# Kernel tuning notes

Hardware: AMD Instinct MI355X
Metric: run time of the kernel (lower is better)

## Reference

```python
import jax, jax.numpy as jnp
import numpy as np

B, L, W, H = 16, 256, 4, 128
N = L + W - 1  # 259
EPS = 1e-6


def setup_inputs() -> dict:
    key = jax.random.key(0)
    k1, k2 = jax.random.split(key)
    x1 = jax.random.normal(k1, (B, 1, N, H), dtype=jnp.float32)
    x2 = jax.random.normal(k2, (B, 1, N, H), dtype=jnp.float32)
    return {"x1": x1, "x2": x2}


def _attention_matrix(x1, x2):
    # x1: (B,1,n,d); x2.permute(0,2,1,3): (B,n,1,d) -> broadcast diff (B,n,n,d)
    diff = x1 - jnp.transpose(x2, (0, 2, 1, 3))
    euclid = jnp.sqrt(jnp.sum(diff * diff, axis=3) + EPS)  # (B,n,n)
    return 1.0 / (euclid + 1.0)


def _wp(x, a):
    # x: (B,1,n,H), a: (B,n) -> weighted sliding-window sum over W positions
    wx = x * a[:, None, :, None]  # (B,1,n,H)
    out = wx[:, :, 0:L, :]
    for k in range(1, W):  # small fixed loop over filter width
        out = out + wx[:, :, k:k + L, :]
    return out  # (B,1,L,H)


def reference(x1, x2):
    att = _attention_matrix(x1, x2)      # (B,n,n)
    x1_a = jnp.sum(att, axis=1)          # (B,n) weight per x1 position
    x2_a = jnp.sum(att, axis=2)          # (B,n) weight per x2 position
    return (_wp(x1, x1_a), _wp(x2, x2_a))
```

## Files before the change

kernel.cpp:

```cpp
#include <hip/hip_runtime.h>
#include <math.h>

#define Bn  16
#define Ln  256
#define Wn  4
#define Hn  128
#define Nn  259
#define EPSF 1e-6f
#define NB  (Bn * Nn)

#define STR 132


__global__ __launch_bounds__(256) void prep(const float* __restrict__ x1,
                                            const float* __restrict__ x2,
                                            float* __restrict__ ws) {
    const int wid  = (blockIdx.x * 256 + threadIdx.x) >> 6;
    const int lane = threadIdx.x & 63;
    if (wid >= 2 * NB) return;
    const float* x = (wid < NB) ? x1 : x2;
    const int    r = (wid < NB) ? wid : wid - NB;
    const float2 v = ((const float2*)(x + (size_t)r * Hn))[lane];
    float s = v.x * v.x + v.y * v.y;
    #pragma unroll
    for (int off = 32; off; off >>= 1) s += __shfl_down(s, off);
    if (lane == 0) {
        ws[wid]          = 0.f;
        ws[2 * NB + wid] = s;
    }
}

__global__ __launch_bounds__(256, 3) void att_sums(const float* __restrict__ x1,
                                                   const float* __restrict__ x2,
                                                   float* __restrict__ ws) {
    __shared__ float x2t[32 * STR];
    __shared__ float x1t[64 * STR];
    __shared__ float nrm[96];

    float*       x1a = ws;
    float*       x2a = ws + NB;
    const float* n1g = ws + 2 * NB;
    const float* n2g = ws + 3 * NB;

    const int b   = blockIdx.z;
    const int i0  = blockIdx.x * 32;
    const int j0  = blockIdx.y * 64;
    const int tid = threadIdx.x;
    const int ti2 = tid >> 4;
    const int tjg = tid & 15;

    const float* __restrict__ x1b = x1 + (size_t)b * Nn * Hn;
    const float* __restrict__ x2b = x2 + (size_t)b * Nn * Hn;

    for (int idx = tid; idx < 32 * 32; idx += 256) {
        const int r = idx >> 5, c = idx & 31;
        float4 v = make_float4(0.f, 0.f, 0.f, 0.f);
        if (i0 + r < Nn) v = ((const float4*)(x2b + (i0 + r) * Hn))[c];
        *((float4*)&x2t[r * STR + c * 4]) = v;
    }
    for (int idx = tid; idx < 64 * 32; idx += 256) {
        const int r = idx >> 5, c = idx & 31;
        float4 v = make_float4(0.f, 0.f, 0.f, 0.f);
        if (j0 + r < Nn) v = ((const float4*)(x1b + (j0 + r) * Hn))[c];
        *((float4*)&x1t[r * STR + c * 4]) = v;
    }
    if (tid < 32)       nrm[tid]      = (i0 + tid < Nn)        ? n2g[b * Nn + i0 + tid]        : 0.f;
    else if (tid < 96)  nrm[tid]      = (j0 + (tid - 32) < Nn) ? n1g[b * Nn + j0 + (tid - 32)] : 0.f;
    __syncthreads();

    float d00 = 0.f, d01 = 0.f, d02 = 0.f, d03 = 0.f;
    float d10 = 0.f, d11 = 0.f, d12 = 0.f, d13 = 0.f;
    const float* arow0 = &x2t[(ti2 * 2    ) * STR];
    const float* arow1 = &x2t[(ti2 * 2 + 1) * STR];
    const float* brow0 = &x1t[(tjg       ) * STR];
    const float* brow1 = &x1t[(tjg + 16  ) * STR];
    const float* brow2 = &x1t[(tjg + 32  ) * STR];
    const float* brow3 = &x1t[(tjg + 48  ) * STR];

    #pragma unroll 4
    for (int h4 = 0; h4 < 32; ++h4) {
        const float4 a0 = *((const float4*)&arow0[h4 * 4]);
        const float4 a1 = *((const float4*)&arow1[h4 * 4]);
        const float4 v0 = *((const float4*)&brow0[h4 * 4]);
        const float4 v1 = *((const float4*)&brow1[h4 * 4]);
        const float4 v2 = *((const float4*)&brow2[h4 * 4]);
        const float4 v3 = *((const float4*)&brow3[h4 * 4]);
        d00 += a0.x * v0.x + a0.y * v0.y + a0.z * v0.z + a0.w * v0.w;
        d01 += a0.x * v1.x + a0.y * v1.y + a0.z * v1.z + a0.w * v1.w;
        d02 += a0.x * v2.x + a0.y * v2.y + a0.z * v2.z + a0.w * v2.w;
        d03 += a0.x * v3.x + a0.y * v3.y + a0.z * v3.z + a0.w * v3.w;
        d10 += a1.x * v0.x + a1.y * v0.y + a1.z * v0.z + a1.w * v0.w;
        d11 += a1.x * v1.x + a1.y * v1.y + a1.z * v1.z + a1.w * v1.w;
        d12 += a1.x * v2.x + a1.y * v2.y + a1.z * v2.z + a1.w * v2.w;
        d13 += a1.x * v3.x + a1.y * v3.y + a1.z * v3.z + a1.w * v3.w;
    }

    const int  ia = i0 + ti2 * 2, ib = ia + 1;
    const bool iva = (ia < Nn), ivb = (ib < Nn);
    const float n2a = nrm[ti2 * 2], n2b = nrm[ti2 * 2 + 1];

    float att0[4], att1[4];
    #pragma unroll
    for (int k = 0; k < 4; ++k) {
        const int   j   = j0 + tjg + 16 * k;
        const bool  jv  = (j < Nn);
        const float n1v = nrm[32 + tjg + 16 * k];
        const float dk0 = (k == 0) ? d00 : (k == 1) ? d01 : (k == 2) ? d02 : d03;
        const float dk1 = (k == 0) ? d10 : (k == 1) ? d11 : (k == 2) ? d12 : d13;
        const float e0  = n2a + n1v - 2.f * dk0 + EPSF;
        const float e1  = n2b + n1v - 2.f * dk1 + EPSF;
        att0[k] = (iva && jv) ? 1.f / (sqrtf(e0) + 1.f) : 0.f;
        att1[k] = (ivb && jv) ? 1.f / (sqrtf(e1) + 1.f) : 0.f;
    }

    float ra = att0[0] + att0[1] + att0[2] + att0[3];
    float rb = att1[0] + att1[1] + att1[2] + att1[3];
    #pragma unroll
    for (int off = 8; off; off >>= 1) {
        ra += __shfl_down(ra, off, 16);
        rb += __shfl_down(rb, off, 16);
    }

    __syncthreads();
    float* colpart = x2t;
    #pragma unroll
    for (int k = 0; k < 4; ++k)
        colpart[ti2 * 68 + tjg + 16 * k] = att0[k] + att1[k];

    if (tjg == 0) {
        if (iva) atomicAdd(&x2a[b * Nn + ia], ra);
        if (ivb) atomicAdd(&x2a[b * Nn + ib], rb);
    }
    __syncthreads();
    if (tid < 64) {
        const int j = j0 + tid;
        if (j < Nn) {
            float cs = 0.f;
            #pragma unroll
            for (int t = 0; t < 16; ++t) cs += colpart[t * 68 + tid];
            atomicAdd(&x1a[b * Nn + j], cs);
        }
    }
}

__global__ __launch_bounds__(256) void wp_kernel(const float* __restrict__ x1,
                                                 const float* __restrict__ x2,
                                                 const float* __restrict__ ws,
                                                 float* __restrict__ out) {
    const int PER = Bn * Ln * Hn / 4;
    int g = blockIdx.x * 256 + threadIdx.x;
    const float* x; const float* a; float4* o; int e;
    if (g < PER) { x = x1; a = ws;      o = (float4*)out;       e = g; }
    else         { x = x2; a = ws + NB; o = (float4*)out + PER; e = g - PER; }

    const int b   = e >> 13;
    const int rem = e & 8191;
    const int l   = rem >> 5;
    const int h4  = rem & 31;

    const float4* xb = (const float4*)(x + (size_t)b * Nn * Hn);
    float4 acc = make_float4(0.f, 0.f, 0.f, 0.f);
    #pragma unroll
    for (int k = 0; k < Wn; ++k) {
        const float  av = a[b * Nn + l + k];
        const float4 xv = xb[(l + k) * (Hn / 4) + h4];
        acc.x += av * xv.x;
        acc.y += av * xv.y;
        acc.z += av * xv.z;
        acc.w += av * xv.w;
    }
    o[e] = acc;
}

extern "C" void kernel_launch(void* const* d_in, const int* in_sizes, int n_in,
                              void* d_out, int out_size, void* d_ws, size_t ws_size,
                              hipStream_t stream) {
    const float* x1 = (const float*)d_in[0];
    const float* x2 = (const float*)d_in[1];
    float* ws = (float*)d_ws;

    prep<<<(2 * NB + 3) / 4, 256, 0, stream>>>(x1, x2, ws);

    dim3 gridA(9, 5, Bn);
    att_sums<<<gridA, 256, 0, stream>>>(x1, x2, ws);

    const int total_f4 = 2 * Bn * Ln * Hn / 4;
    wp_kernel<<<total_f4 / 256, 256, 0, stream>>>(x1, x2, ws, (float*)d_out);
}
```

Baseline: 77.56 us.

## Compute pairwise dot products with bf16 MFMA instead of fp32 FMA

The prep kernel now also converts x1 and x2 to bf16 copies in the workspace and computes the squared norms from those rounded values. The attention kernel is replaced by one that stages bf16 tiles in shared memory and uses 16x16x32 bf16 matrix-core instructions to form the 64x64 dot-product tiles. It then reduces row and column sums with shuffles and atomics. This cuts FMA work and shared-memory traffic, but loses precision in the distance computation, and catastrophic cancellation in norm minus twice the dot product could hurt accuracy.

Result: faster. 70.54 us (-9.1%).

```diff
diff --git a/kernel.cpp b/kernel.cpp
--- a/kernel.cpp
+++ b/kernel.cpp
@@ -1,4 +1,5 @@
 #include <hip/hip_runtime.h>
+#include <hip/hip_bf16.h>
 #include <math.h>
 
 #define Bn  16
@@ -9,7 +10,8 @@
 #define EPSF 1e-6f
 #define NB  (Bn * Nn)
 
-#define STR 132
+typedef float f32x4 __attribute__((ext_vector_type(4)));
+typedef short s16x8 __attribute__((ext_vector_type(8)));
 
 
 __global__ __launch_bounds__(256) void prep(const float* __restrict__ x1,
@@ -18,10 +20,18 @@
     const int wid  = (blockIdx.x * 256 + threadIdx.x) >> 6;
     const int lane = threadIdx.x & 63;
     if (wid >= 2 * NB) return;
-    const float* x = (wid < NB) ? x1 : x2;
-    const int    r = (wid < NB) ? wid : wid - NB;
+    const bool one = (wid < NB);
+    const float* x = one ? x1 : x2;
+    const int    r = one ? wid : wid - NB;
     const float2 v = ((const float2*)(x + (size_t)r * Hn))[lane];
-    float s = v.x * v.x + v.y * v.y;
+    union { __hip_bfloat16 h; unsigned short u; } c0, c1;
+    c0.h = __float2bfloat16(v.x);
+    c1.h = __float2bfloat16(v.y);
+    unsigned short* xb = (unsigned short*)(ws + 4 * NB) + (one ? 0 : (size_t)NB * Hn);
+    ((unsigned int*)(xb + (size_t)r * Hn))[lane] =
+        (unsigned int)c0.u | ((unsigned int)c1.u << 16);
+    const float a0 = __bfloat162float(c0.h), a1 = __bfloat162float(c1.h);
+    float s = a0 * a0 + a1 * a1;
     #pragma unroll
     for (int off = 32; off; off >>= 1) s += __shfl_down(s, off);
     if (lane == 0) {
@@ -30,116 +40,75 @@
     }
 }
 
-__global__ __launch_bounds__(256, 3) void att_sums(const float* __restrict__ x1,
-                                                   const float* __restrict__ x2,
-                                                   float* __restrict__ ws) {
-    __shared__ float x2t[32 * STR];
-    __shared__ float x1t[64 * STR];
-    __shared__ float nrm[96];
+__global__ __launch_bounds__(256) void att_mfma(float* __restrict__ ws) {
+    __shared__ unsigned short As[64 * 136];
+    __shared__ unsigned short Bs[64 * 136];
+    __shared__ float n2s[64], n1s[64];
 
     float*       x1a = ws;
     float*       x2a = ws + NB;
     const float* n1g = ws + 2 * NB;
     const float* n2g = ws + 3 * NB;
+    const unsigned short* xb1 = (const unsigned short*)(ws + 4 * NB);
+    const unsigned short* xb2 = xb1 + (size_t)NB * Hn;
 
-    const int b   = blockIdx.z;
-    const int i0  = blockIdx.x * 32;
-    const int j0  = blockIdx.y * 64;
+    const int i0 = blockIdx.x * 64, j0 = blockIdx.y * 64, b = blockIdx.z;
     const int tid = threadIdx.x;
-    const int ti2 = tid >> 4;
-    const int tjg = tid & 15;
 
-    const float* __restrict__ x1b = x1 + (size_t)b * Nn * Hn;
-    const float* __restrict__ x2b = x2 + (size_t)b * Nn * Hn;
-
-    for (int idx = tid; idx < 32 * 32; idx += 256) {
-        const int r = idx >> 5, c = idx & 31;
-        float4 v = make_float4(0.f, 0.f, 0.f, 0.f);
-        if (i0 + r < Nn) v = ((const float4*)(x2b + (i0 + r) * Hn))[c];
-        *((float4*)&x2t[r * STR + c * 4]) = v;
+    for (int idx = tid; idx < 1024; idx += 256) {
+        const int r = idx >> 4, c = idx & 15;
+        uint4 va = make_uint4(0, 0, 0, 0), vb = va;
+        if (i0 + r < Nn) va = ((const uint4*)(xb2 + (size_t)(b * Nn + i0 + r) * Hn))[c];
+        if (j0 + r < Nn) vb = ((const uint4*)(xb1 + (size_t)(b * Nn + j0 + r) * Hn))[c];
+        *((uint4*)&As[r * 136 + c * 8]) = va;
+        *((uint4*)&Bs[r * 136 + c * 8]) = vb;
     }
-    for (int idx = tid; idx < 64 * 32; idx += 256) {
-        const int r = idx >> 5, c = idx & 31;
-        float4 v = make_float4(0.f, 0.f, 0.f, 0.f);
-        if (j0 + r < Nn) v = ((const float4*)(x1b + (j0 + r) * Hn))[c];
-        *((float4*)&x1t[r * STR + c * 4]) = v;
-    }
-    if (tid < 32)       nrm[tid]      = (i0 + tid < Nn)        ? n2g[b * Nn + i0 + tid]        : 0.f;
-    else if (tid < 96)  nrm[tid]      = (j0 + (tid - 32) < Nn) ? n1g[b * Nn + j0 + (tid - 32)] : 0.f;
+    if (tid < 64)       n2s[tid]      = (i0 + tid < Nn)        ? n2g[b * Nn + i0 + tid]        : 0.f;
+    else if (tid < 128) n1s[tid - 64] = (j0 + (tid - 64) < Nn) ? n1g[b * Nn + j0 + (tid - 64)] : 0.f;
     __syncthreads();
 
-    float d00 = 0.f, d01 = 0.f, d02 = 0.f, d03 = 0.f;
-    float d10 = 0.f, d11 = 0.f, d12 = 0.f, d13 = 0.f;
-    const float* arow0 = &x2t[(ti2 * 2    ) * STR];
-    const float* arow1 = &x2t[(ti2 * 2 + 1) * STR];
-    const float* brow0 = &x1t[(tjg       ) * STR];
-    const float* brow1 = &x1t[(tjg + 16  ) * STR];
-    const float* brow2 = &x1t[(tjg + 32  ) * STR];
-    const float* brow3 = &x1t[(tjg + 48  ) * STR];
+    const int w = tid >> 6, lane = tid & 63;
+    const int rsel = lane & 15, q = lane >> 4;
 
-    #pragma unroll 4
-    for (int h4 = 0; h4 < 32; ++h4) {
-        const float4 a0 = *((const float4*)&arow0[h4 * 4]);
-        const float4 a1 = *((const float4*)&arow1[h4 * 4]);
-        const float4 v0 = *((const float4*)&brow0[h4 * 4]);
-        const float4 v1 = *((const float4*)&brow1[h4 * 4]);
-        const float4 v2 = *((const float4*)&brow2[h4 * 4]);
-        const float4 v3 = *((const float4*)&brow3[h4 * 4]);
-        d00 += a0.x * v0.x + a0.y * v0.y + a0.z * v0.z + a0.w * v0.w;
-        d01 += a0.x * v1.x + a0.y * v1.y + a0.z * v1.z + a0.w * v1.w;
-        d02 += a0.x * v2.x + a0.y * v2.y + a0.z * v2.z + a0.w * v2.w;
-        d03 += a0.x * v3.x + a0.y * v3.y + a0.z * v3.z + a0.w * v3.w;
-        d10 += a1.x * v0.x + a1.y * v0.y + a1.z * v0.z + a1.w * v0.w;
-        d11 += a1.x * v1.x + a1.y * v1.y + a1.z * v1.z + a1.w * v1.w;
-        d12 += a1.x * v2.x + a1.y * v2.y + a1.z * v2.z + a1.w * v2.w;
-        d13 += a1.x * v3.x + a1.y * v3.y + a1.z * v3.z + a1.w * v3.w;
+    f32x4 acc[4] = {{0,0,0,0}, {0,0,0,0}, {0,0,0,0}, {0,0,0,0}};
+    const unsigned short* arow = &As[(w * 16 + rsel) * 136 + q * 8];
+    const unsigned short* brow = &Bs[rsel * 136 + q * 8];
+    #pragma unroll
+    for (int s = 0; s < 4; ++s) {
+        const s16x8 af = *((const s16x8*)(arow + s * 32));
+        #pragma unroll
+        for (int t = 0; t < 4; ++t) {
+            const s16x8 bf = *((const s16x8*)(brow + t * 16 * 136 + s * 32));
+            acc[t] = __builtin_amdgcn_mfma_f32_16x16x32_bf16(af, bf, acc[t], 0, 0, 0);
+        }
     }
 
-    const int  ia = i0 + ti2 * 2, ib = ia + 1;
-    const bool iva = (ia < Nn), ivb = (ib < Nn);
-    const float n2a = nrm[ti2 * 2], n2b = nrm[ti2 * 2 + 1];
-
-    float att0[4], att1[4];
+    float rowacc[4] = {0.f, 0.f, 0.f, 0.f};
     #pragma unroll
-    for (int k = 0; k < 4; ++k) {
-        const int   j   = j0 + tjg + 16 * k;
+    for (int t = 0; t < 4; ++t) {
+        const int   j   = j0 + t * 16 + rsel;
         const bool  jv  = (j < Nn);
-        const float n1v = nrm[32 + tjg + 16 * k];
-        const float dk0 = (k == 0) ? d00 : (k == 1) ? d01 : (k == 2) ? d02 : d03;
-        const float dk1 = (k == 0) ? d10 : (k == 1) ? d11 : (k == 2) ? d12 : d13;
-        const float e0  = n2a + n1v - 2.f * dk0 + EPSF;
-        const float e1  = n2b + n1v - 2.f * dk1 + EPSF;
-        att0[k] = (iva && jv) ? 1.f / (sqrtf(e0) + 1.f) : 0.f;
-        att1[k] = (ivb && jv) ? 1.f / (sqrtf(e1) + 1.f) : 0.f;
+        const float n1v = n1s[t * 16 + rsel];
+        float cp = 0.f;
+        #pragma unroll
+        for (int reg = 0; reg < 4; ++reg) {
+            const int   i   = i0 + w * 16 + q * 4 + reg;
+            const float e   = fmaf(-2.f, acc[t][reg], n2s[w * 16 + q * 4 + reg] + n1v + EPSF);
+            const float att = ((i < Nn) && jv) ? 1.f / (sqrtf(e) + 1.f) : 0.f;
+            rowacc[reg] += att;
+            cp          += att;
+        }
+        cp += __shfl_xor(cp, 16);
+        cp += __shfl_xor(cp, 32);
+        if (q == 0 && jv) atomicAdd(&x1a[b * Nn + j], cp);
     }
-
-    float ra = att0[0] + att0[1] + att0[2] + att0[3];
-    float rb = att1[0] + att1[1] + att1[2] + att1[3];
     #pragma unroll
-    for (int off = 8; off; off >>= 1) {
-        ra += __shfl_down(ra, off, 16);
-        rb += __shfl_down(rb, off, 16);
-    }
-
-    __syncthreads();
-    float* colpart = x2t;
-    #pragma unroll
-    for (int k = 0; k < 4; ++k)
-        colpart[ti2 * 68 + tjg + 16 * k] = att0[k] + att1[k];
-
-    if (tjg == 0) {
-        if (iva) atomicAdd(&x2a[b * Nn + ia], ra);
-        if (ivb) atomicAdd(&x2a[b * Nn + ib], rb);
-    }
-    __syncthreads();
-    if (tid < 64) {
-        const int j = j0 + tid;
-        if (j < Nn) {
-            float cs = 0.f;
-            #pragma unroll
-            for (int t = 0; t < 16; ++t) cs += colpart[t * 68 + tid];
-            atomicAdd(&x1a[b * Nn + j], cs);
-        }
+    for (int reg = 0; reg < 4; ++reg) {
+        float rs = rowacc[reg];
+        #pragma unroll
+        for (int off = 8; off; off >>= 1) rs += __shfl_down(rs, off, 16);
+        const int i = i0 + w * 16 + q * 4 + reg;
+        if (rsel == 0 && i < Nn) atomicAdd(&x2a[b * Nn + i], rs);
     }
 }
 
@@ -181,8 +150,8 @@
 
     prep<<<(2 * NB + 3) / 4, 256, 0, stream>>>(x1, x2, ws);
 
-    dim3 gridA(9, 5, Bn);
-    att_sums<<<gridA, 256, 0, stream>>>(x1, x2, ws);
+    dim3 gridA(5, 5, Bn);
+    att_mfma<<<gridA, 256, 0, stream>>>(ws);
 
     const int total_f4 = 2 * Bn * Ln * Hn / 4;
     wp_kernel<<<total_f4 / 256, 256, 0, stream>>>(x1, x2, ws, (float*)d_out);
```
